# Performance work log

Hardware: AMD Instinct MI355X
Metric: run time of the kernel (lower is better)

The kernel has to match this reference:

```python
import jax, jax.numpy as jnp
import numpy as np

B, L, C, H, K, P = 64, 2048, 128, 128, 64, 336
NUM_BLOCKS = 4
EPS = 1e-5


def _revin_norm(x):
    mean = jnp.mean(x, axis=1, keepdims=True)
    std = jnp.sqrt(jnp.var(x, axis=1, keepdims=True) + EPS)
    return (x - mean) / std, mean, std


def _bn(x, gamma, beta, ch_axis):
    # training-mode BatchNorm1d: stats over all axes except ch_axis
    axes = tuple(i for i in range(x.ndim) if i != ch_axis)
    mean = jnp.mean(x, axis=axes, keepdims=True)
    var = jnp.var(x, axis=axes, keepdims=True)
    shp = [1] * x.ndim
    shp[ch_axis] = -1
    return (x - mean) / jnp.sqrt(var + EPS) * gamma.reshape(shp) + beta.reshape(shp)


def _mixer_block(x, bn_t_g, bn_t_b, lin_t_w, lin_t_b, bn_f_g, bn_f_b,
                 lin_f1_w, lin_f1_b, lin_f2_w, lin_f2_b):
    # timestep mixer: BN treats seq dim as channels, Linear over seq dim
    y = _bn(x, bn_t_g, bn_t_b, 1)                       # [B,L,C]
    y = jnp.swapaxes(y, 1, 2)                           # [B,C,L]
    y = jax.nn.gelu(y @ lin_t_w + lin_t_b, approximate=False)
    y = jnp.swapaxes(y, 1, 2)
    x = x + y
    # feature mixer: BN over channel dim, 2-layer MLP over features
    y = jnp.swapaxes(x, 1, 2)                           # [B,C,L]
    y = _bn(y, bn_f_g, bn_f_b, 1)
    y = jnp.swapaxes(y, 1, 2)                           # [B,L,C]
    y = jax.nn.gelu(y @ lin_f1_w + lin_f1_b, approximate=False)
    y = y @ lin_f2_w + lin_f2_b
    return x + y


def _forward(x, bern_u, cluster_embeds, wq_w, wq_b, wk_w, wk_b, wv_w, wv_b,
             cm_w1, cm_b1, cm_w2, cm_b2, tm_w1, tm_b1, tm_w2, tm_b2,
             bn_t_g, bn_t_b, lin_t_w, lin_t_b, bn_f_g, bn_f_b,
             lin_f1_w, lin_f1_b, lin_f2_w, lin_f2_b, out_w, out_b):
    xn, _, _ = _revin_norm(x)                           # [B,L,C]
    # channel MLP -> token embeddings h_i
    h = jax.nn.relu(xn @ cm_w1 + cm_b1) @ cm_w2 + cm_b2  # [B,L,H]
    # cosine-similarity soft routing to codebook
    hn = h / (jnp.linalg.norm(h, axis=-1, keepdims=True) + 1e-8)
    cn = cluster_embeds / (jnp.linalg.norm(cluster_embeds, axis=-1, keepdims=True) + 1e-8)
    p = jax.nn.softmax(jnp.einsum('blh,kh->blk', hn, cn), axis=-1)   # [B,L,K]
    M = (bern_u < p).astype(x.dtype)                    # bernoulli sample via external uniforms
    # exp-attention between cluster queries and token keys, masked by M
    Q = cluster_embeds @ wq_w + wq_b                    # [K,H]
    Km = h @ wk_w + wk_b                                # [B,L,H]
    V = h @ wv_w + wv_b                                 # [B,L,H]
    scores = jnp.einsum('kh,blh->bkl', Q, Km) / jnp.sqrt(jnp.asarray(H, x.dtype))
    aw = jax.nn.softmax(jnp.exp(scores) * jnp.swapaxes(M, 1, 2), axis=-1)  # [B,K,L]
    ao = jnp.einsum('bkl,blh->bkh', aw, V)              # [B,K,H]
    upd = ao * jnp.mean(p, axis=1)[:, :, None]          # prob-weighted cluster update
    new_cluster_embeds = jnp.mean(upd, axis=0)          # [K,H] (EMA-style copy target)
    # temporal module on channel embeddings
    h2 = jax.nn.relu(h @ tm_w1 + tm_b1) @ tm_w2 + tm_b2  # [B,L,H], H==C
    z, mean2, std2 = _revin_norm(h2)                    # second 'norm' overwrites stats
    for _ in range(NUM_BLOCKS):
        z = _mixer_block(z, bn_t_g, bn_t_b, lin_t_w, lin_t_b,
                         bn_f_g, bn_f_b, lin_f1_w, lin_f1_b, lin_f2_w, lin_f2_b)
    y = jnp.swapaxes(jnp.swapaxes(z, 1, 2) @ out_w + out_b, 1, 2)    # [B,P,C]
    y = y * std2 + mean2                                # denorm with second-call stats
    return y, new_cluster_embeds


def setup_inputs() -> dict:
    key = jax.random.key(0)
    ks = iter(jax.random.split(key, 40))

    def lin_w(fan_in, shape):
        return jax.random.uniform(next(ks), shape, jnp.float32, -1.0, 1.0) / np.sqrt(fan_in).astype(np.float32)

    return {
        'x': jax.random.normal(next(ks), (B, L, C), jnp.float32),
        'bern_u': jax.random.uniform(next(ks), (B, L, K), jnp.float32),
        'cluster_embeds': jax.random.normal(next(ks), (K, H), jnp.float32),
        'wq_w': lin_w(H, (H, H)), 'wq_b': lin_w(H, (H,)),
        'wk_w': lin_w(H, (H, H)), 'wk_b': lin_w(H, (H,)),
        'wv_w': lin_w(H, (H, H)), 'wv_b': lin_w(H, (H,)),
        'cm_w1': lin_w(C, (C, H)), 'cm_b1': lin_w(C, (H,)),
        'cm_w2': lin_w(H, (H, H)), 'cm_b2': lin_w(H, (H,)),
        'tm_w1': lin_w(H, (H, H)), 'tm_b1': lin_w(H, (H,)),
        'tm_w2': lin_w(H, (H, H)), 'tm_b2': lin_w(H, (H,)),
        'bn_t_g': jnp.ones((L,), jnp.float32), 'bn_t_b': jnp.zeros((L,), jnp.float32),
        'lin_t_w': lin_w(L, (L, L)), 'lin_t_b': lin_w(L, (L,)),
        'bn_f_g': jnp.ones((C,), jnp.float32), 'bn_f_b': jnp.zeros((C,), jnp.float32),
        'lin_f1_w': lin_w(C, (C, H)), 'lin_f1_b': lin_w(C, (H,)),
        'lin_f2_w': lin_w(H, (H, C)), 'lin_f2_b': lin_w(H, (C,)),
        'out_w': lin_w(L, (L, P)), 'out_b': lin_w(L, (P,)),
    }


def reference(x, bern_u, cluster_embeds, wq_w, wq_b, wk_w, wk_b, wv_w, wv_b,
              cm_w1, cm_b1, cm_w2, cm_b2, tm_w1, tm_b1, tm_w2, tm_b2,
              bn_t_g, bn_t_b, lin_t_w, lin_t_b, bn_f_g, bn_f_b,
              lin_f1_w, lin_f1_b, lin_f2_w, lin_f2_b, out_w, out_b):
    return _forward(x, bern_u, cluster_embeds, wq_w, wq_b, wk_w, wk_b, wv_w, wv_b,
                    cm_w1, cm_b1, cm_w2, cm_b2, tm_w1, tm_b1, tm_w2, tm_b2,
                    bn_t_g, bn_t_b, lin_t_w, lin_t_b, bn_f_g, bn_f_b,
                    lin_f1_w, lin_f1_b, lin_f2_w, lin_f2_b, out_w, out_b)
```

## Files before the change

kernel.cpp:

```cpp
#include <hip/hip_runtime.h>
#include <math.h>

#define BB 64
#define LL 2048
#define CC 128
#define HH 128
#define KK 64
#define PP 336
#define EPSf 1e-5f

typedef __attribute__((ext_vector_type(8))) short short8v;
typedef __attribute__((ext_vector_type(4))) float float4v;

__device__ inline ushort f2bf(float f) {
    union { float f; unsigned u; } v; v.f = f;
    unsigned r = (v.u + 0x7FFFu + ((v.u >> 16) & 1u)) >> 16;
    return (ushort)r;
}
__device__ inline float bf2f(ushort h) {
    union { unsigned u; float f; } v; v.u = ((unsigned)h) << 16;
    return v.f;
}

__device__ inline float fast_gelu(float v) {
// ... 283 lines not shown
    __shared__ ushort Xlo[PREC ? 128 : 1][72];
    __shared__ ushort Bh[128][72];
    __shared__ ushort Bl[PREC ? 128 : 1][72];
    int tid = threadIdx.x;
    int m0 = blockIdx.x * 128;
    int noff = (NORM == 1) ? (m0 / LL) * normStride : 0;
    int w = tid >> 6, lane = tid & 63;
    int wm = (w >> 1) * 64, wn = (w & 1) * 64;
    int col = lane & 15, kq = lane >> 4;

    float4v acc[4][4];
    #pragma unroll
    for (int i = 0; i < 4; ++i)
        #pragma unroll
        for (int j = 0; j < 4; ++j) acc[i][j] = (float4v){0.f, 0.f, 0.f, 0.f};

    for (int kt = 0; kt < 2; ++kt) {
        __syncthreads();
        #pragma unroll
        for (int it = 0; it < 4; ++it) {
            int q = tid + it * 256;
            int row = q >> 3, k0 = (q & 7) * 8;
            int kg = kt * 64 + k0;
            const float* ap = A + (size_t)(m0 + row) * 128 + kg;
            float vv[8];
            *(float4*)&vv[0] = *(const float4*)ap;
            *(float4*)&vv[4] = *(const float4*)(ap + 4);
            ushort hi[8], lo[8];
            #pragma unroll
            for (int j = 0; j < 8; ++j) {
                float v = vv[j];
                if (NORM == 1) v = (v - nmu[noff + kg + j]) * ns[noff + kg + j];
                if (NORM == 2) v = (v - nmu[kg + j]) * ns[kg + j] + nt[kg + j];
                ushort h = f2bf(v);
                hi[j] = h;
                if (PREC) lo[j] = f2bf(v - bf2f(h));
            }
            *(short8v*)&Xhi[row][k0] = *(short8v*)hi;
            if (PREC) *(short8v*)&Xlo[row][k0] = *(short8v*)lo;
        }
        #pragma unroll
        for (int it = 0; it < 4; ++it) {
            int q = tid + it * 256;
            int row = q >> 3, k0 = (q & 7) * 8;
            *(short8v*)&Bh[row][k0] =
                *(const short8v*)(W1h + (size_t)row * 128 + kt * 64 + k0);
            if (PREC)
                *(short8v*)&Bl[row][k0] =
                    *(const short8v*)(W1l + (size_t)row * 128 + kt * 64 + k0);
        }
        __syncthreads();
        #pragma unroll
        for (int ksub = 0; ksub < 2; ++ksub) {
            short8v ah[4], al[4], bh[4], bl[4];
            #pragma unroll
            for (int mf = 0; mf < 4; ++mf) {
                ah[mf] = *(const short8v*)&Xhi[wm + mf * 16 + col][ksub * 32 + kq * 8];
                if (PREC) al[mf] = *(const short8v*)&Xlo[wm + mf * 16 + col][ksub * 32 + kq * 8];
            }
            #pragma unroll
            for (int nf = 0; nf < 4; ++nf) {
                bh[nf] = *(const short8v*)&Bh[wn + nf * 16 + col][ksub * 32 + kq * 8];
                if (PREC) bl[nf] = *(const short8v*)&Bl[wn + nf * 16 + col][ksub * 32 + kq * 8];
            }
            #pragma unroll
            for (int mf = 0; mf < 4; ++mf)
                #pragma unroll
                for (int nf = 0; nf < 4; ++nf)
                    acc[mf][nf] = __builtin_amdgcn_mfma_f32_16x16x32_bf16(
                        ah[mf], bh[nf], acc[mf][nf], 0, 0, 0);
            if (PREC) {
                #pragma unroll
                for (int mf = 0; mf < 4; ++mf)
                    #pragma unroll
                    for (int nf = 0; nf < 4; ++nf)
                        acc[mf][nf] = __builtin_amdgcn_mfma_f32_16x16x32_bf16(
                            ah[mf], bl[nf], acc[mf][nf], 0, 0, 0);
                #pragma unroll
                for (int mf = 0; mf < 4; ++mf)
                    #pragma unroll
                    for (int nf = 0; nf < 4; ++nf)
                        acc[mf][nf] = __builtin_amdgcn_mfma_f32_16x16x32_bf16(
                            al[mf], bh[nf], acc[mf][nf], 0, 0, 0);
            }
        }
    }

    float4v acc2[4][4];
    #pragma unroll
    for (int i = 0; i < 4; ++i)
        #pragma unroll
        for (int j = 0; j < 4; ++j) acc2[i][j] = (float4v){0.f, 0.f, 0.f, 0.f};

    for (int kt2 = 0; kt2 < 2; ++kt2) {
        __syncthreads();
        if ((wn >> 6) == kt2) {
            #pragma unroll
            for (int nf = 0; nf < 4; ++nf) {
                float bn = b1v[wn + nf * 16 + col];
                #pragma unroll
                for (int mf = 0; mf < 4; ++mf) {
                    #pragma unroll
                    for (int r = 0; r < 4; ++r) {
                        float v = acc[mf][nf][r] + bn;
                        if (ACT1 == 1) v = fmaxf(v, 0.f);
                        if (ACT1 == 2) v = fast_gelu(v);
                        int row = wm + mf * 16 + kq * 4 + r;
                        int c2 = nf * 16 + col;
                        ushort h = f2bf(v);
                        Xhi[row][c2] = h;
                        if (PREC) Xlo[row][c2] = f2bf(v - bf2f(h));
                    }
                }
            }
        }
        #pragma unroll
        for (int it = 0; it < 4; ++it) {
            int q = tid + it * 256;
            int row = q >> 3, k0 = (q & 7) * 8;
            *(short8v*)&Bh[row][k0] =
                *(const short8v*)(W2h + (size_t)row * 128 + kt2 * 64 + k0);
            if (PREC)
                *(short8v*)&Bl[row][k0] =
                    *(const short8v*)(W2l + (size_t)row * 128 + kt2 * 64 + k0);
        }
        __syncthreads();
        #pragma unroll
        for (int ksub = 0; ksub < 2; ++ksub) {
            short8v ah[4], al[4], bh[4], bl[4];
            #pragma unroll
            for (int mf = 0; mf < 4; ++mf) {
                ah[mf] = *(const short8v*)&Xhi[wm + mf * 16 + col][ksub * 32 + kq * 8];
                if (PREC) al[mf] = *(const short8v*)&Xlo[wm + mf * 16 + col][ksub * 32 + kq * 8];
            }
            #pragma unroll
            for (int nf = 0; nf < 4; ++nf) {
                bh[nf] = *(const short8v*)&Bh[wn + nf * 16 + col][ksub * 32 + kq * 8];
                if (PREC) bl[nf] = *(const short8v*)&Bl[wn + nf * 16 + col][ksub * 32 + kq * 8];
            }
            #pragma unroll
            for (int mf = 0; mf < 4; ++mf)
                #pragma unroll
                for (int nf = 0; nf < 4; ++nf)
                    acc2[mf][nf] = __builtin_amdgcn_mfma_f32_16x16x32_bf16(
                        ah[mf], bh[nf], acc2[mf][nf], 0, 0, 0);
            if (PREC) {
                #pragma unroll
                for (int mf = 0; mf < 4; ++mf)
                    #pragma unroll
                    for (int nf = 0; nf < 4; ++nf)
                        acc2[mf][nf] = __builtin_amdgcn_mfma_f32_16x16x32_bf16(
                            ah[mf], bl[nf], acc2[mf][nf], 0, 0, 0);
                #pragma unroll
                for (int mf = 0; mf < 4; ++mf)
                    #pragma unroll
                    for (int nf = 0; nf < 4; ++nf)
                        acc2[mf][nf] = __builtin_amdgcn_mfma_f32_16x16x32_bf16(
                            al[mf], bh[nf], acc2[mf][nf], 0, 0, 0);
            }
        }
    }

    int rbase = kq * 4;
    float rs_[4][4];
    float rq_[4][4];
    float cs_[4], cq_[4];
    if (EP2 == 1 || EP2 == 3) {
        #pragma unroll
        for (int a = 0; a < 4; ++a)
            #pragma unroll
            for (int b = 0; b < 4; ++b) { rs_[a][b] = 0.f; rq_[a][b] = 0.f; }
    }
    if (EP2 == 2) {
        #pragma unroll
        for (int a = 0; a < 4; ++a) { cs_[a] = 0.f; cq_[a] = 0.f; }
    }
    #pragma unroll
    for (int nf = 0; nf < 4; ++nf) {
        int n = wn + nf * 16 + col;
        float bn = b2v[n];
        #pragma unroll
        for (int mf = 0; mf < 4; ++mf) {
            #pragma unroll
            for (int r = 0; r < 4; ++r) {
                int m = m0 + wm + mf * 16 + rbase + r;
                float v = acc2[mf][nf][r] + bn;
                if (ACT2 == 1) v = fmaxf(v, 0.f);
                if (ACT2 == 2) v = fast_gelu(v);
                if (EP2 == 1) {
                    float fin = Out[(size_t)m * 128 + n] + v;
                    Out[(size_t)m * 128 + n] = fin;
                    rs_[mf][r] += fin;
                    rq_[mf][r] += fin * fin;
                } else {
                    Out[(size_t)m * 128 + n] = v;
                    if (EP2 == 2) { cs_[nf] += v; cq_[nf] += v * v; }
                    if (EP2 == 3) rq_[mf][r] += v * v;
                }
            }
        }
    }
    if (EP2 == 1) {
        #pragma unroll
        for (int mf = 0; mf < 4; ++mf)
            #pragma unroll
            for (int r = 0; r < 4; ++r) {
                float s = rs_[mf][r], q = rq_[mf][r];
                #pragma unroll
                for (int o = 1; o <= 8; o <<= 1) {
                    s += __shfl_xor(s, o);
                    q += __shfl_xor(q, o);
                }
                rs_[mf][r] = s; rq_[mf][r] = q;
            }
        __syncthreads();
        float* sred = (float*)&Xhi[0][0];
        float* qred = sred + 256;
        if (col == 0) {
            #pragma unroll
            for (int mf = 0; mf < 4; ++mf)
                #pragma unroll
                for (int r = 0; r < 4; ++r) {
                    int row = wm + mf * 16 + kq * 4 + r;
                    sred[row * 2 + (wn >> 6)] = rs_[mf][r];
                    qred[row * 2 + (wn >> 6)] = rq_[mf][r];
                }
        }
        __syncthreads();
        if (tid < 128) {
            rsum[(size_t)m0 + tid] = sred[tid * 2] + sred[tid * 2 + 1];
            rsq[(size_t)m0 + tid]  = qred[tid * 2] + qred[tid * 2 + 1];
        }
    }
    if (EP2 == 3) {
        #pragma unroll
        for (int mf = 0; mf < 4; ++mf)
            #pragma unroll
            for (int r = 0; r < 4; ++r) {
                float q = rq_[mf][r];
                #pragma unroll
                for (int o = 1; o <= 8; o <<= 1) q += __shfl_xor(q, o);
                rq_[mf][r] = q;
            }
        __syncthreads();
        float* qred = (float*)&Xhi[0][0];
        if (col == 0) {
            #pragma unroll
            for (int mf = 0; mf < 4; ++mf)
                #pragma unroll
                for (int r = 0; r < 4; ++r) {
                    int row = wm + mf * 16 + kq * 4 + r;
                    qred[row * 2 + (wn >> 6)] = rq_[mf][r];
                }
        }
        __syncthreads();
        if (tid < 128)
            rsq[(size_t)m0 + tid] = qred[tid * 2] + qred[tid * 2 + 1];
    }
    if (EP2 == 2) {
        #pragma unroll
        for (int nf = 0; nf < 4; ++nf) {
            #pragma unroll
            for (int o = 16; o <= 32; o <<= 1) {
                cs_[nf] += __shfl_xor(cs_[nf], o);
                cq_[nf] += __shfl_xor(cq_[nf], o);
            }
        }
        __syncthreads();
        float* colS = (float*)&Xhi[0][0];
        float* colQ = colS + 256;
        if (kq == 0) {
            #pragma unroll
            for (int nf = 0; nf < 4; ++nf) {
                int n = wn + nf * 16 + col;
                colS[(wm >> 6) * 128 + n] = cs_[nf];
                colQ[(wm >> 6) * 128 + n] = cq_[nf];
            }
        }
        __syncthreads();
        if (tid < 128) {
            rsum[(size_t)blockIdx.x * 256 + tid] = colS[tid] + colS[128 + tid];
            rsum[(size_t)blockIdx.x * 256 + 128 + tid] = colQ[tid] + colQ[128 + tid];
        }
    }
}

__global__ void wsplit_kernel(const float* __restrict__ W, ushort* __restrict__ Whi,
                              ushort* __restrict__ Wlo) {
    __shared__ float t[32][33];
    int k0 = blockIdx.x * 32, n0 = blockIdx.y * 32;
    int tx = threadIdx.x, ty = threadIdx.y;
    for (int i = ty; i < 32; i += 8)
        t[i][tx] = W[(size_t)(k0 + i) * 128 + n0 + tx];
    __syncthreads();
    for (int i = ty; i < 32; i += 8) {
        float v = t[tx][i];
        ushort h = f2bf(v);
        Whi[(size_t)(n0 + i) * 128 + k0 + tx] = h;
        Wlo[(size_t)(n0 + i) * 128 + k0 + tx] = f2bf(v - bf2f(h));
    }
}

__global__ __launch_bounds__(512, 1)
void mfma_ts2_kernel(const ushort* __restrict__ A, const ushort* __restrict__ W,
                     const float* __restrict__ bias, float* Z,
                     float* __restrict__ bnfP) {
    extern __shared__ __align__(16) ushort smem2[];
    float (*Ol)[260] = (float(*)[260])smem2;

    int bid = blockIdx.x;
    int swz = (bid & 7) * 32 + (bid >> 3);
    int n0 = (swz & 7) * 256;
    int m0 = (swz >> 3) * 256;

    int tid = threadIdx.x;
    int w = tid >> 6, lane = tid & 63;
    int wm = (w >> 2) * 128, wn = (w & 3) * 64;
    int col = lane & 15, kq = lane >> 4;
    int srow = lane >> 3;
    int scol = ((lane & 7) ^ srow) << 3;
    int xr = (col & 7) << 4;

    float4v acc[8][4];
    #pragma unroll
    for (int i = 0; i < 8; ++i)
        #pragma unroll
        for (int j = 0; j < 4; ++j) acc[i][j] = (float4v){0.f, 0.f, 0.f, 0.f};

    const int kTiles = 32;
    auto stage = [&](int kt2, int bsel) {
        ushort* Ab = smem2 + bsel * 32768;
        ushort* Bb = Ab + 16384;
        int kb = kt2 << 6;
        #pragma unroll
        for (int it = 0; it < 4; ++it) {
            int rb = w * 32 + it * 8;
            async16(A + (size_t)(m0 + rb + srow) * LL + kb + scol, Ab + (rb << 6));
            async16(W + (size_t)(n0 + rb + srow) * LL + kb + scol, Bb + (rb << 6));
        }
    };

    stage(0, 0);
    __syncthreads();
    for (int kt = 0; kt < kTiles; ++kt) {
        int cur = kt & 1;
        const ushort* Ac = smem2 + cur * 32768;
        const ushort* Bc = Ac + 16384;
        if (kt + 1 < kTiles) stage(kt + 1, cur ^ 1);
        __builtin_amdgcn_s_setprio(1);
        #pragma unroll
        for (int ksub = 0; ksub < 2; ++ksub) {
            int cswz = (((ksub << 6) + (kq << 4)) ^ xr) >> 1;
            short8v af[8], bf[4];
            #pragma unroll
            for (int mf = 0; mf < 8; ++mf)
                af[mf] = *(const short8v*)(Ac + (wm + mf * 16 + col) * 64 + cswz);
            #pragma unroll
            for (int nf = 0; nf < 4; ++nf)
                bf[nf] = *(const short8v*)(Bc + (wn + nf * 16 + col) * 64 + cswz);
            #pragma unroll
            for (int mf = 0; mf < 8; ++mf)
                #pragma unroll
                for (int nf = 0; nf < 4; ++nf)
                    acc[mf][nf] = __builtin_amdgcn_mfma_f32_16x16x32_bf16(
                        af[mf], bf[nf], acc[mf][nf], 0, 0, 0);
        }
        __builtin_amdgcn_s_setprio(0);
        __syncthreads();
    }

    int b0 = m0 >> 7;
    float cs[16], cq[16];
    #pragma unroll
    for (int j = 0; j < 16; ++j) { cs[j] = 0.f; cq[j] = 0.f; }
    int nloc = tid >> 4, c0 = (tid & 15) * 16;
    int bb = b0 + (c0 >> 7);
    int ccc = c0 & 127;
    #pragma unroll
    for (int q = 0; q < 8; ++q) {
        __syncthreads();
        #pragma unroll
        for (int nf = 0; nf < 4; ++nf) {
            int gnl = wn + nf * 16;
            if ((gnl >> 5) != q) continue;
            int gn = n0 + gnl + col;
            float bn = bias[gn];
            int nl = gnl - q * 32 + col;
            #pragma unroll
            for (int mf = 0; mf < 8; ++mf)
                #pragma unroll
                for (int r = 0; r < 4; ++r) {
                    float v = acc[mf][nf][r] + bn;
                    v = fast_gelu(v);
                    Ol[nl][wm + mf * 16 + kq * 4 + r] = v;
                }
        }
        __syncthreads();
        int gn = n0 + q * 32 + nloc;
        float* zr = Z + ((size_t)bb * LL + gn) * CC + ccc;
        #pragma unroll
        for (int i = 0; i < 4; ++i) {
            float4 v = *(float4*)&Ol[nloc][c0 + i * 4];
            float4 o = *(float4*)(zr + i * 4);
            v.x += o.x; v.y += o.y; v.z += o.z; v.w += o.w;
            *(float4*)(zr + i * 4) = v;
            cs[i * 4 + 0] += v.x; cs[i * 4 + 1] += v.y;
            cs[i * 4 + 2] += v.z; cs[i * 4 + 3] += v.w;
            cq[i * 4 + 0] += v.x * v.x; cq[i * 4 + 1] += v.y * v.y;
            cq[i * 4 + 2] += v.z * v.z; cq[i * 4 + 3] += v.w * v.w;
        }
    }
    __syncthreads();
    float* sred = (float*)smem2;
    float* qred = sred + 8192;
    #pragma unroll
    for (int j = 0; j < 16; ++j) {
        sred[nloc * 256 + c0 + j] = cs[j];
        qred[nloc * 256 + c0 + j] = cq[j];
    }
    __syncthreads();
    if (tid < 128) {
        float a = 0.f;
        for (int r = 0; r < 32; ++r)
            a += sred[r * 256 + tid] + sred[r * 256 + 128 + tid];
        bnfP[(size_t)bid * 256 + tid] = a;
    } else if (tid < 256) {
        int c = tid - 128;
        float a = 0.f;
        for (int r = 0; r < 32; ++r)
            a += qred[r * 256 + c] + qred[r * 256 + 128 + c];
        bnfP[(size_t)bid * 256 + 128 + c] = a;
    }
}

template <int EPM>
__global__ __launch_bounds__(256)
void mfma_gemm_kernel(const ushort* __restrict__ A, const ushort* __restrict__ W,
                      const float* __restrict__ bias, float* Z,
                      int N, int Kd, int LDO, int nx, int nwg,
                      const float* __restrict__ epS, const float* __restrict__ epM,
                      float* __restrict__ bnfP) {
    __shared__ __align__(16) ushort smem[32768];
    float (*Ol)[132] = (float(*)[132])smem;

    int bid = blockIdx.x;
    int cpx = nwg >> 3;
    int swz = (bid & 7) * cpx + (bid >> 3);
    int n0 = (swz % nx) * 128;
    int m0 = (swz / nx) * 128;

    int tid = threadIdx.x;
    int w = tid >> 6, lane = tid & 63;
    int wm = (w >> 1) * 64, wn = (w & 1) * 64;
    int col = lane & 15, kq = lane >> 4;

    int srow = lane >> 3;
    int scol = ((lane & 7) ^ srow) << 3;
    int xr = (col & 7) << 4;

    float4v acc[4][4];
    #pragma unroll
    for (int i = 0; i < 4; ++i)
        #pragma unroll
        for (int j = 0; j < 4; ++j) acc[i][j] = (float4v){0.f, 0.f, 0.f, 0.f};

    int kTiles = Kd >> 6;

    #pragma unroll
    for (int it = 0; it < 4; ++it) {
        int rb = (w << 5) + (it << 3);
        async16(A + (size_t)(m0 + rb + srow) * Kd + scol, smem + (rb << 6));
    }
    #pragma unroll
    for (int it = 0; it < 4; ++it) {
        int rb = (w << 5) + (it << 3);
        async16(W + (size_t)(n0 + rb + srow) * Kd + scol, smem + 8192 + (rb << 6));
    }
    __syncthreads();

    for (int kt = 0; kt < kTiles; ++kt) {
        int cur = kt & 1;
        ushort* Ac = smem + (cur << 14);
        ushort* Bc = Ac + 8192;
        if (kt + 1 < kTiles) {
            ushort* An = smem + ((cur ^ 1) << 14);
            ushort* Bn = An + 8192;
            int kb = (kt + 1) << 6;
            #pragma unroll
            for (int it = 0; it < 4; ++it) {
                int rb = (w << 5) + (it << 3);
                async16(A + (size_t)(m0 + rb + srow) * Kd + kb + scol, An + (rb << 6));
            }
            #pragma unroll
            for (int it = 0; it < 4; ++it) {
                int rb = (w << 5) + (it << 3);
                async16(W + (size_t)(n0 + rb + srow) * Kd + kb + scol, Bn + (rb << 6));
            }
        }
        __builtin_amdgcn_s_setprio(1);
        #pragma unroll
        for (int ksub = 0; ksub < 2; ++ksub) {
            int cswz = (((ksub << 6) + (kq << 4)) ^ xr) >> 1;
            short8v af[4], bf[4];
            #pragma unroll
            for (int mf = 0; mf < 4; ++mf)
                af[mf] = *(const short8v*)(Ac + (wm + mf * 16 + col) * 64 + cswz);
            #pragma unroll
            for (int nf = 0; nf < 4; ++nf)
                bf[nf] = *(const short8v*)(Bc + (wn + nf * 16 + col) * 64 + cswz);
            #pragma unroll
            for (int mf = 0; mf < 4; ++mf)
                #pragma unroll
                for (int nf = 0; nf < 4; ++nf)
                    acc[mf][nf] = __builtin_amdgcn_mfma_f32_16x16x32_bf16(
                        af[mf], bf[nf], acc[mf][nf], 0, 0, 0);
        }
        __builtin_amdgcn_s_setprio(0);
        __syncthreads();
    }

    int b = m0 >> 7;
    float cs[16], cq[16];
    if (EPM == 1) {
        #pragma unroll
        for (int k2 = 0; k2 < 16; ++k2) { cs[k2] = 0.f; cq[k2] = 0.f; }
    }
    #pragma unroll
    for (int q = 0; q < 4; ++q) {
        __syncthreads();
        #pragma unroll
        for (int nf = 0; nf < 4; ++nf) {
            int gnl = wn + nf * 16;
            if ((gnl >> 5) != q) continue;
            int gn = n0 + gnl + col;
            float bn = (EPM == 2 && gn >= N) ? 0.f : bias[gn];
            int nl = gnl - q * 32 + col;
            #pragma unroll
            for (int mf = 0; mf < 4; ++mf) {
                #pragma unroll
                for (int r = 0; r < 4; ++r) {
                    float v = acc[mf][nf][r] + bn;
                    if (EPM == 1) v = fast_gelu(v);
                    Ol[nl][wm + mf * 16 + kq * 4 + r] = v;
                }
            }
        }
        __syncthreads();
        int nloc = tid >> 3, c0 = (tid & 7) * 16;
        int gn = n0 + q * 32 + nloc;
        if ((EPM == 2 || EPM == 3) && gn >= N) continue;
        float* zr;
        if (EPM == 3)
            zr = Z + (((size_t)(m0 >> 11) * 64 + gn) * 2048) + (m0 & 2047) + c0;
        else
            zr = Z + ((size_t)b * LDO + gn) * CC + c0;
        #pragma unroll
        for (int i = 0; i < 4; ++i) {
            float4 v = *(float4*)&Ol[nloc][c0 + i * 4];
            if (EPM == 1) {
                float4 o = *(float4*)(zr + i * 4);
                v.x += o.x; v.y += o.y; v.z += o.z; v.w += o.w;
                *(float4*)(zr + i * 4) = v;
                cs[i * 4 + 0] += v.x; cs[i * 4 + 1] += v.y;
                cs[i * 4 + 2] += v.z; cs[i * 4 + 3] += v.w;
                cq[i * 4 + 0] += v.x * v.x; cq[i * 4 + 1] += v.y * v.y;
                cq[i * 4 + 2] += v.z * v.z; cq[i * 4 + 3] += v.w * v.w;
            } else if (EPM == 2) {
                int mb = m0 + c0 + i * 4;
                float4 s4 = *(const float4*)(epS + mb);
                float4 m4 = *(const float4*)(epM + mb);
                v.x = v.x * s4.x + m4.x; v.y = v.y * s4.y + m4.y;
                v.z = v.z * s4.z + m4.z; v.w = v.w * s4.w + m4.w;
                *(float4*)(zr + i * 4) = v;
            } else {
                *(float4*)(zr + i * 4) = v;
            }
        }
    }
    if (EPM == 1) {
        __syncthreads();
        float* sred = (float*)smem;
        float* qred = sred + 4096;
        int rrow = tid >> 3, cb = (tid & 7) * 16;
        #pragma unroll
        for (int k2 = 0; k2 < 16; ++k2) {
            sred[rrow * 128 + cb + k2] = cs[k2];
            qred[rrow * 128 + cb + k2] = cq[k2];
        }
        __syncthreads();
        if (tid < 128) {
            float a = 0.f;
            for (int r = 0; r < 32; ++r) a += sred[r * 128 + tid];
            bnfP[(size_t)bid * 256 + tid] = a;
        } else {
            int c = tid - 128;
            float a = 0.f;
            for (int r = 0; r < 32; ++r) a += qred[r * 128 + c];
            bnfP[(size_t)bid * 256 + 128 + c] = a;
        }
    }
}

__global__ void wtrans_kernel(const float* __restrict__ W, ushort* __restrict__ WT,
                              int Kd, int N) {
    __shared__ float t[32][33];
    int k0 = blockIdx.x * 32, n0 = blockIdx.y * 32;
    int tx = threadIdx.x, ty = threadIdx.y;
    for (int i = ty; i < 32; i += 8) {
        int n = n0 + tx;
        t[i][tx] = (n < N) ? W[(size_t)(k0 + i) * N + n] : 0.f;
    }
    __syncthreads();
    for (int i = ty; i < 32; i += 8)
        WT[(size_t)(n0 + i) * Kd + k0 + tx] = f2bf(t[tx][i]);
}

__global__ void cn_split_kernel(const float* __restrict__ ce, ushort* __restrict__ ch,
                                ushort* __restrict__ cl) {
    int k = blockIdx.x, h = threadIdx.x;
    if (k >= KK) {
        ch[(size_t)k * 128 + h] = 0;
        cl[(size_t)k * 128 + h] = 0;
        return;
    }
    __shared__ float sh[128];
    float v = ce[(size_t)k * HH + h];
    sh[h] = v * v;
    __syncthreads();
    for (int o = 64; o >= 1; o >>= 1) {
        if (h < o) sh[h] += sh[h + o];
        __syncthreads();
    }
    float nv = v / (sqrtf(sh[0]) + 1e-8f);
    ushort hh = f2bf(nv);
    ch[(size_t)k * 128 + h] = hh;
    cl[(size_t)k * 128 + h] = f2bf(nv - bf2f(hh));
}

__global__ void qprime_kernel(const float* __restrict__ Q, const float* __restrict__ wk_w,
                              const float* __restrict__ wk_b, ushort* __restrict__ qpb,
                              float* __restrict__ qbp) {
    int k = blockIdx.x;
    int hp = threadIdx.x;
    if (k >= KK) {
        qpb[(size_t)k * HH + hp] = 0;
        if (hp == 0) qbp[k] = 0.f;
        return;
    }
    __shared__ float qrow[128];
    __shared__ float red[128];
    qrow[hp] = Q[(size_t)k * HH + hp];
    __syncthreads();
    float s = 0.f;
    for (int h = 0; h < HH; ++h) s = fmaf(qrow[h], wk_w[(size_t)hp * HH + h], s);
    const float rs = 0.088388347648318447f;
    qpb[(size_t)k * HH + hp] = f2bf(s * rs);
    red[hp] = qrow[hp] * wk_b[hp];
    __syncthreads();
    for (int o = 64; o >= 1; o >>= 1) {
        if (hp < o) red[hp] += red[hp + o];
        __syncthreads();
    }
    if (hp == 0) qbp[k] = red[0] * rs;
}

__global__ __launch_bounds__(256)
void pmask_kernel(const float* __restrict__ sp, const float* __restrict__ rn,
                  const float* __restrict__ bern, unsigned char* __restrict__ Mt,
                  float* __restrict__ ppart) {
    int b = blockIdx.y;
    int l0 = blockIdx.x * 32;
// ... 38 lines not shown
__global__ __launch_bounds__(256)
void aw_kernel(float* __restrict__ S, const unsigned char* __restrict__ Mt) {
    size_t base = (size_t)blockIdx.x * LL;
    int tid = threadIdx.x;
    float t[8];
    float mx = -1e30f;
    #pragma unroll
    for (int i = 0; i < 8; ++i) {
        int l = tid + i * 256;
        float v = expf(S[base + l]) * (float)Mt[base + l];
        t[i] = v;
        mx = fmaxf(mx, v);
    }
    __shared__ float shA[4];
    __shared__ float shB[4];
    #pragma unroll
    for (int o = 32; o >= 1; o >>= 1) mx = fmaxf(mx, __shfl_xor(mx, o));
    if ((tid & 63) == 0) shA[tid >> 6] = mx;
    __syncthreads();
    mx = fmaxf(fmaxf(shA[0], shA[1]), fmaxf(shA[2], shA[3]));
    float e[8];
    float sum = 0.f;
    #pragma unroll
    for (int i = 0; i < 8; ++i) { e[i] = expf(t[i] - mx); sum += e[i]; }
    #pragma unroll
    for (int o = 32; o >= 1; o >>= 1) sum += __shfl_xor(sum, o);
    if ((tid & 63) == 0) shB[tid >> 6] = sum;
    __syncthreads();
    sum = (shB[0] + shB[1]) + (shB[2] + shB[3]);
    float inv = 1.f / sum;
    #pragma unroll
    for (int i = 0; i < 8; ++i) S[base + tid + i * 256] = e[i] * inv;
}

__global__ __launch_bounds__(256)
void awh_part_kernel(const float* __restrict__ AWs, const float* __restrict__ hmat,
                     float* __restrict__ part) {
    __shared__ float AT[32][64];
    __shared__ float VT[32][128];
    int b = blockIdx.y, sp = blockIdx.x;
    int tid = threadIdx.x;
    int tx = tid & 15, ty = tid >> 4;
    float acc[4][8] = {};
    const float* Ab = AWs + (size_t)b * KK * LL + sp * 512;
    const float* Vb = hmat + ((size_t)b * LL + sp * 512) * HH;
    for (int lt = 0; lt < 512; lt += 32) {
        __syncthreads();
        #pragma unroll
        for (int it = 0; it < 2; ++it) {
            int q = tid + it * 256;
            int row = q >> 3;
            int lq = (q & 7) << 2;
            float4 v = *(const float4*)(Ab + (size_t)row * LL + lt + lq);
            AT[lq][row] = v.x; AT[lq + 1][row] = v.y;
            AT[lq + 2][row] = v.z; AT[lq + 3][row] = v.w;
        }
        #pragma unroll
        for (int it = 0; it < 4; ++it) {
            int q = tid + it * 256;
            int lr = q >> 5;
            int hc = (q & 31) << 2;
            *(float4*)&VT[lr][hc] = *(const float4*)(Vb + (size_t)(lt + lr) * HH + hc);
        }
        __syncthreads();
        #pragma unroll
        for (int l = 0; l < 32; ++l) {
            float av[4], vv[8];
            *(float4*)&av[0] = *(const float4*)&AT[l][ty * 4];
            *(float4*)&vv[0] = *(const float4*)&VT[l][tx * 4];
            *(float4*)&vv[4] = *(const float4*)&VT[l][64 + tx * 4];
            #pragma unroll
            for (int i = 0; i < 4; ++i)
                #pragma unroll
                for (int j = 0; j < 8; ++j)
                    acc[i][j] = fmaf(av[i], vv[j], acc[i][j]);
        }
    }
    #pragma unroll
    for (int i = 0; i < 4; ++i) {
        int k = ty * 4 + i;
        #pragma unroll
        for (int jj = 0; jj < 8; jj += 4) {
            int h = (jj ? 64 + tx * 4 : tx * 4);
            float o[4];
            #pragma unroll
            for (int j = 0; j < 4; ++j) o[j] = acc[i][jj + j];
            *(float4*)(part + (((size_t)b * 4 + sp) * KK + k) * HH + h) = *(float4*)o;
        }
    }
}

__global__ void awh_reduce_kernel(const float* __restrict__ part, float* __restrict__ awh) {
    int bk = blockIdx.x, h = threadIdx.x;
    int b = bk >> 6, k = bk & 63;
    float s = 0.f;
    #pragma unroll
    for (int sp = 0; sp < 4; ++sp)
        s += part[(((size_t)b * 4 + sp) * KK + k) * HH + h];
    awh[(size_t)bk * HH + h] = s;
}

__global__ void newce_kernel(const float* __restrict__ ao, const float* __restrict__ pm,
                             float* __restrict__ outTail) {
    int k = blockIdx.x, h = threadIdx.x;
    float s = 0.f;
    for (int b = 0; b < BB; ++b)
        s += ao[((size_t)b * KK + k) * HH + h] * pm[b * KK + k];
    outTail[(size_t)k * HH + h] = s * (1.f / BB);
}

__global__ void revin_apply_kernel(const float* __restrict__ in, float* __restrict__ out,
                                   const float* __restrict__ mu, const float* __restrict__ rs,
                                   float* __restrict__ rsum, float* __restrict__ rsq) {
    int b = blockIdx.y;
    size_t base = (size_t)b * LL * CC + (size_t)blockIdx.x * 8192;
    int c0 = (threadIdx.x * 4) & 127;
    int lane = threadIdx.x & 63;
    float4 m4 = *(const float4*)(mu + b * CC + c0);
    float4 r4 = *(const float4*)(rs + b * CC + c0);
    #pragma unroll
    for (int j = 0; j < 8; ++j) {
        float4 v = *(const float4*)(in + base + threadIdx.x * 4 + j * 1024);
        v.x = (v.x - m4.x) * r4.x; v.y = (v.y - m4.y) * r4.y;
        v.z = (v.z - m4.z) * r4.z; v.w = (v.w - m4.w) * r4.w;
        *(float4*)(out + base + threadIdx.x * 4 + j * 1024) = v;
        float s = v.x + v.y + v.z + v.w;
        float q = v.x * v.x + v.y * v.y + v.z * v.z + v.w * v.w;
        #pragma unroll
        for (int o = 1; o <= 16; o <<= 1) {
            s += __shfl_xor(s, o);
            q += __shfl_xor(q, o);
        }
        if ((lane & 31) == 0) {
            size_t row = (base + (size_t)threadIdx.x * 4 + (size_t)j * 1024) >> 7;
            rsum[row] = s;
            rsq[row] = q;
        }
    }
}

__global__ void bnt_final_kernel(const float* __restrict__ rsum, const float* __restrict__ rsq,
                                 float* __restrict__ mu, float* __restrict__ rv) {
    int l = blockIdx.x * 256 + threadIdx.x;
    float s = 0.f, q = 0.f;
    for (int b = 0; b < BB; ++b) {
        s += rsum[(size_t)b * LL + l];
        q += rsq[(size_t)b * LL + l];
    }
    float m = s * (1.f / (BB * CC));
    float var = q * (1.f / (BB * CC)) - m * m;
    var = fmaxf(var, 0.f);
    mu[l] = m;
    rv[l] = 1.f / sqrtf(var + EPSf);
}

template <bool DO_BN>
__global__ __launch_bounds__(256)
void transpose_bn_kernel(const float* __restrict__ in, ushort* __restrict__ out,
                         const float* __restrict__ mu, const float* __restrict__ rv,
                         const float* __restrict__ g, const float* __restrict__ be) {
    __shared__ ushort tile[32][72];
    int l0 = blockIdx.x * 64, c0 = blockIdx.y * 32, b = blockIdx.z;
    int t = threadIdx.x;
    const float* ib = in + ((size_t)b * LL + l0) * CC + c0;
    #pragma unroll
    for (int it = 0; it < 2; ++it) {
        int idx = t + it * 256;
        int row = idx >> 3;
        int c = (idx & 7) * 4;
        float4 v = *(const float4*)(ib + (size_t)row * CC + c);
        if (DO_BN) {
            int l = l0 + row;
            float sc = rv[l] * g[l];
            float m = mu[l], bb = be[l];
            v.x = (v.x - m) * sc + bb; v.y = (v.y - m) * sc + bb;
            v.z = (v.z - m) * sc + bb; v.w = (v.w - m) * sc + bb;
        }
        tile[c    ][row] = f2bf(v.x);
        tile[c + 1][row] = f2bf(v.y);
        tile[c + 2][row] = f2bf(v.z);
        tile[c + 3][row] = f2bf(v.w);
    }
    __syncthreads();
    int cc = t >> 3, l8 = (t & 7) * 8;
    ushort* ob = out + (size_t)b * CC * LL + (size_t)(c0 + cc) * LL + l0 + l8;
    *(uint4*)ob = *(const uint4*)&tile[cc][l8];
}

__global__ void bnf_mid_kernel(const float* __restrict__ part, float* __restrict__ mid,
                               int cnt) {
    int gblk = blockIdx.x, t = threadIdx.x;
    float s = 0.f;
    for (int i = 0; i < cnt; ++i)
        s += part[(size_t)(gblk * cnt + i) * 256 + t];
    mid[(size_t)gblk * 256 + t] = s;
}

__global__ void bnf_final_kernel(const float* __restrict__ mid, const float* __restrict__ g,
                                 const float* __restrict__ be, float* __restrict__ mu,
                                 float* __restrict__ sA, float* __restrict__ tA) {
    int c = threadIdx.x;
    float s = 0.f, s2 = 0.f;
    #pragma unroll
    for (int i = 0; i < 64; ++i) {
        s += mid[(size_t)i * 256 + c];
        s2 += mid[(size_t)i * 256 + 128 + c];
    }
    float m = s / (float)(BB * LL);
    float var = s2 / (float)(BB * LL) - m * m;
    var = fmaxf(var, 0.f);
    float rvv = 1.f / sqrtf(var + EPSf);
    mu[c] = m;
    sA[c] = rvv * g[c];
    tA[c] = be[c];
}

extern "C" void kernel_launch(void* const* d_in, const int* in_sizes, int n_in,
                              void* d_out, int out_size, void* d_ws, size_t ws_size,
                              hipStream_t stream) {
    const float* x     = (const float*)d_in[0];
    const float* bern  = (const float*)d_in[1];
    const float* ce    = (const float*)d_in[2];
    const float* wq_w  = (const float*)d_in[3];
    const float* wq_b  = (const float*)d_in[4];
    const float* wk_w  = (const float*)d_in[5];
    const float* wk_b  = (const float*)d_in[6];
    const float* wv_w  = (const float*)d_in[7];
    const float* wv_b  = (const float*)d_in[8];
    const float* cm_w1 = (const float*)d_in[9];
    const float* cm_b1 = (const float*)d_in[10];
    const float* cm_w2 = (const float*)d_in[11];
    const float* cm_b2 = (const float*)d_in[12];
    const float* tm_w1 = (const float*)d_in[13];
    const float* tm_b1 = (const float*)d_in[14];
    const float* tm_w2 = (const float*)d_in[15];
    const float* tm_b2 = (const float*)d_in[16];
    const float* bn_t_g = (const float*)d_in[17];
    const float* bn_t_b = (const float*)d_in[18];
    const float* lin_t_w = (const float*)d_in[19];
    const float* lin_t_b = (const float*)d_in[20];
    const float* bn_f_g = (const float*)d_in[21];
    const float* bn_f_b = (const float*)d_in[22];
    const float* f1_w  = (const float*)d_in[23];
    const float* f1_b  = (const float*)d_in[24];
    const float* f2_w  = (const float*)d_in[25];
    const float* f2_b  = (const float*)d_in[26];
    const float* out_w = (const float*)d_in[27];
    const float* out_b = (const float*)d_in[28];
    (void)in_sizes; (void)n_in; (void)out_size;

    float* y = (float*)d_out;
    float* ceOut = y + (size_t)BB * PP * CC;

    float* ws = (float*)d_ws;
    size_t off = 0;
    auto alloc = [&](size_t n) { float* p = ws + off; off += n; return p; };
    float* mean1  = alloc(BB * CC);
    float* rstd1  = alloc(BB * CC);
    float* std1   = alloc(BB * CC);
    float* mean2  = alloc(BB * CC);
    float* rstd2  = alloc(BB * CC);
    float* std2   = alloc(BB * CC);
    float* bnmu   = alloc(LL);
    float* bnrv   = alloc(LL);
    float* bfpart = alloc(1024 * 256);
    float* bfmid  = alloc(64 * 256);
    float* bfmu   = alloc(CC);
    float* bfs    = alloc(CC);
    float* bft    = alloc(CC);
    float* cxpart = alloc(BB * 8 * 256);
    float* cpart2 = alloc(1024 * 256);
    float* qbuf   = alloc(KK * HH);
    ushort* qpb   = (ushort*)alloc(128 * 128 / 2);
    float* qbp    = alloc(128);
    ushort* cnbh  = (ushort*)alloc(8192);
    ushort* cnbl  = (ushort*)alloc(8192);
    float* rn     = alloc((size_t)BB * LL);
    float* rsum   = alloc((size_t)BB * LL);
    float* rsq    = alloc((size_t)BB * LL);
    float* ppart  = alloc((size_t)BB * (LL / 32) * KK);
    float* pmean  = alloc(BB * KK);
    float* awhprt = alloc((size_t)BB * 4 * KK * HH);
    float* awh    = alloc((size_t)BB * KK * HH);
    float* aobuf  = alloc((size_t)BB * KK * HH);
    ushort* wsp   = (ushort*)alloc(7 * 2 * 16384 / 2);
    ushort* wtT   = (ushort*)alloc((size_t)LL * LL / 2);
    ushort* owT   = (ushort*)alloc((size_t)384 * LL / 2);
    float* S      = alloc((size_t)BB * KK * LL);
    float* buf0   = alloc((size_t)BB * LL * CC);
    float* buf2   = alloc((size_t)BB * LL * CC);
    unsigned char* Mt = (unsigned char*)(ws + off);
    ushort* abf = (ushort*)S;
    ushort* hb  = (ushort*)buf0;
    (void)ws_size;

    auto whi = [&](int i) { return wsp + (size_t)i * 2 * 16384; };
    auto wlo = [&](int i) { return wsp + (size_t)i * 2 * 16384 + 16384; };

    const int ML = BB * LL;
    dim3 tb(32, 8);
    dim3 tgrid(LL / 64, CC / 32, BB);
    dim3 wsg(4, 4);

    bool useTs2 =
        (hipFuncSetAttribute((const void*)mfma_ts2_kernel,
                             hipFuncAttributeMaxDynamicSharedMemorySize,
                             131072) == hipSuccess);

    wtrans_kernel<<<dim3(LL / 32, LL / 32), tb, 0, stream>>>(lin_t_w, wtT, LL, LL);
    wtrans_kernel<<<dim3(LL / 32, 12), tb, 0, stream>>>(out_w, owT, LL, PP);
    wsplit_kernel<<<wsg, tb, 0, stream>>>(cm_w1, whi(0), wlo(0));
    wsplit_kernel<<<wsg, tb, 0, stream>>>(cm_w2, whi(1), wlo(1));
    wsplit_kernel<<<wsg, tb, 0, stream>>>(tm_w1, whi(2), wlo(2));
    wsplit_kernel<<<wsg, tb, 0, stream>>>(tm_w2, whi(3), wlo(3));
    wsplit_kernel<<<wsg, tb, 0, stream>>>(f1_w, whi(4), wlo(4));
    wsplit_kernel<<<wsg, tb, 0, stream>>>(f2_w, whi(5), wlo(5));
    wsplit_kernel<<<wsg, tb, 0, stream>>>(wv_w, whi(6), wlo(6));

    colstats_part_kernel<<<dim3(8, BB), 256, 0, stream>>>(x, cxpart);
    colstats_final_kernel<<<dim3(BB), dim3(128), 0, stream>>>(cxpart, mean1, rstd1, std1);
    mfma_sq2_kernel<1, 1, 0, 3, 1><<<dim3(ML / 128), 256, 0, stream>>>(
        x, whi(0), wlo(0), cm_b1, whi(1), wlo(1), cm_b2, buf2, mean1, rstd1, nullptr, CC,
        nullptr, rsq);
    rn_final_kernel<<<dim3(ML / 256), 256, 0, stream>>>(rsq, rn);
    gemm_kernel<<<dim3(1, 1), 256, 0, stream>>>(ce, wq_w, wq_b, qbuf,
        KK, HH, HH, HH, HH, HH);
    qprime_kernel<<<dim3(128), dim3(128), 0, stream>>>(qbuf, wk_w, wk_b, qpb, qbp);
    cn_split_kernel<<<dim3(128), dim3(128), 0, stream>>>(ce, cnbh, cnbl);
    mfma_sq_kernel<0, 0, 2><<<dim3(ML / 128), 256, 0, stream>>>(
        buf2, cnbh, cnbl, nullptr, S, nullptr, nullptr, nullptr, 0, hb);
    pmask_kernel<<<dim3(LL / 32, BB), 256, 0, stream>>>(S, rn, bern, Mt, ppart);
    pmean_final_kernel<<<dim3(BB), dim3(64), 0, stream>>>(ppart, pmean);
    mfma_gemm_kernel<3><<<dim3(1024), 256, 0, stream>>>(
        hb, qpb, qbp, S, KK, 128, 0, 1, 1024, nullptr, nullptr, nullptr);
    aw_kernel<<<dim3(BB * KK), 256, 0, stream>>>(S, Mt);
    awh_part_kernel<<<dim3(4, BB), 256, 0, stream>>>(S, buf2, awhprt);
    awh_reduce_kernel<<<dim3(BB * KK), dim3(128), 0, stream>>>(awhprt, awh);
    mfma_sq_kernel<0, 0, 0><<<dim3((BB * KK) / 128), 256, 0, stream>>>(
        awh, whi(6), wlo(6), wv_b, aobuf, nullptr, nullptr, nullptr, 0, nullptr);
    newce_kernel<<<dim3(KK), dim3(128), 0, stream>>>(aobuf, pmean, ceOut);
    mfma_sq2_kernel<0, 1, 0, 2, 1><<<dim3(ML / 128), 256, 0, stream>>>(
        buf2, whi(2), wlo(2), tm_b1, whi(3), wlo(3), tm_b2, buf0,
        nullptr, nullptr, nullptr, 0, cpart2, nullptr);
    colstats2_final_kernel<<<dim3(BB), dim3(128), 0, stream>>>(cpart2, mean2, rstd2, std2);
    revin_apply_kernel<<<dim3(32, BB), 256, 0, stream>>>(buf0, buf2, mean2, rstd2, rsum, rsq);
    for (int blkI = 0; blkI < 4; ++blkI) {
        bnt_final_kernel<<<dim3(8), 256, 0, stream>>>(rsum, rsq, bnmu, bnrv);
        transpose_bn_kernel<true><<<tgrid, 256, 0, stream>>>(buf2, abf, bnmu, bnrv, bn_t_g, bn_t_b);
        if (useTs2) {
            mfma_ts2_kernel<<<dim3(256), 512, 131072, stream>>>(
                abf, wtT, lin_t_b, buf2, bfpart);
            bnf_mid_kernel<<<dim3(64), 256, 0, stream>>>(bfpart, bfmid, 4);
        } else {
            mfma_gemm_kernel<1><<<dim3(1024), 256, 0, stream>>>(
                abf, wtT, lin_t_b, buf2, LL, LL, LL, 16, 1024, nullptr, nullptr, bfpart);
            bnf_mid_kernel<<<dim3(64), 256, 0, stream>>>(bfpart, bfmid, 16);
        }
        bnf_final_kernel<<<dim3(1), dim3(128), 0, stream>>>(bfmid, bn_f_g, bn_f_b, bfmu, bfs, bft);
        mfma_sq2_kernel<2, 2, 0, 1, 0><<<dim3(ML / 128), 256, 0, stream>>>(
            buf2, whi(4), wlo(4), f1_b, whi(5), wlo(5), f2_b, buf2, bfmu, bfs, bft, 0,
            rsum, rsq);
    }
    transpose_bn_kernel<false><<<tgrid, 256, 0, stream>>>(buf2, abf,
        nullptr, nullptr, nullptr, nullptr);
    mfma_gemm_kernel<2><<<dim3(192), 256, 0, stream>>>(
        abf, owT, out_b, y, PP, LL, PP, 3, 192, std2, mean2, nullptr);
}
```

Measured before the change: 1.357 ms.

## Use 4-stage async pipeline with half-k tiles in time-mixing GEMM

Restructures the main timestep-mixing GEMM mainloop from a double-buffered 64-wide k tile into a four-slot ring of 32-wide k stages, kept three stages ahead, with explicit vmcnt waits and a single barrier per stage. It also changes the LDS layout to pack two rows per 64-element line with a new XOR swizzle, so fragment reads avoid bank conflicts. The aim is to hide global-load latency better and drop the trailing __syncthreads. The risk is that it relies on exact vmcnt counting and a ring-slot reuse distance for correctness.

```diff
diff --git a/kernel.cpp b/kernel.cpp
--- a/kernel.cpp
+++ b/kernel.cpp
@@ -609,7 +609,7 @@
 }
 
 __global__ __launch_bounds__(512, 1)
-void mfma_ts2_kernel(const ushort* __restrict__ A, const ushort* __restrict__ W,
+void mfma_ts3_kernel(const ushort* __restrict__ A, const ushort* __restrict__ W,
                      const float* __restrict__ bias, float* Z,
                      float* __restrict__ bnfP) {
     extern __shared__ __align__(16) ushort smem2[];
@@ -624,9 +624,15 @@
     int w = tid >> 6, lane = tid & 63;
     int wm = (w >> 2) * 128, wn = (w & 3) * 64;
     int col = lane & 15, kq = lane >> 4;
-    int srow = lane >> 3;
-    int scol = ((lane & 7) ^ srow) << 3;
-    int xr = (col & 7) << 4;
+
+    int l3 = lane >> 3;
+    int u0 = (lane & 7) ^ l3;
+    int urow = l3 * 2 + (u0 >> 2);
+    int ucol = (u0 & 3) * 8;
+
+    int uoff = ((((col & 1) << 2) | kq) ^ (col >> 1)) * 8;
+    int rA2b = (wm >> 1) + (col >> 1);
+    int rB2b = (wn >> 1) + (col >> 1);
 
     float4v acc[8][4];
     #pragma unroll
@@ -634,46 +640,44 @@
         #pragma unroll
         for (int j = 0; j < 4; ++j) acc[i][j] = (float4v){0.f, 0.f, 0.f, 0.f};
 
-    const int kTiles = 32;
-    auto stage = [&](int kt2, int bsel) {
-        ushort* Ab = smem2 + bsel * 32768;
-        ushort* Bb = Ab + 16384;
-        int kb = kt2 << 6;
-        #pragma unroll
-        for (int it = 0; it < 4; ++it) {
-            int rb = w * 32 + it * 8;
-            async16(A + (size_t)(m0 + rb + srow) * LL + kb + scol, Ab + (rb << 6));
-            async16(W + (size_t)(n0 + rb + srow) * LL + kb + scol, Bb + (rb << 6));
+    auto stage = [&](int q) {
+        int kb = (q >> 1) * 64 + (q & 1) * 32;
+        ushort* base = smem2 + (q & 3) * 16384;
+        #pragma unroll
+        for (int it = 0; it < 2; ++it) {
+            int R0 = w * 16 + it * 8;
+            async16(A + (size_t)(m0 + R0 * 2 + urow) * LL + kb + ucol,
+                    base + R0 * 64);
+            async16(W + (size_t)(n0 + R0 * 2 + urow) * LL + kb + ucol,
+                    base + 8192 + R0 * 64);
         }
     };
 
-    stage(0, 0);
-    __syncthreads();
-    for (int kt = 0; kt < kTiles; ++kt) {
-        int cur = kt & 1;
-        const ushort* Ac = smem2 + cur * 32768;
-        const ushort* Bc = Ac + 16384;
-        if (kt + 1 < kTiles) stage(kt + 1, cur ^ 1);
+    stage(0); stage(1); stage(2);
+
+    for (int P = 0; P < 64; ++P) {
+        if (P < 62)       asm volatile("s_waitcnt vmcnt(8)" ::: "memory");
+        else if (P == 62) asm volatile("s_waitcnt vmcnt(4)" ::: "memory");
+        else              asm volatile("s_waitcnt vmcnt(0)" ::: "memory");
+        __builtin_amdgcn_s_barrier();
+        __builtin_amdgcn_sched_barrier(0);
+        if (P < 61) stage(P + 3);
+        const ushort* base = smem2 + (size_t)(P & 3) * 16384;
+        short8v af[8], bf4[4];
+        #pragma unroll
+        for (int mf = 0; mf < 8; ++mf)
+            af[mf] = *(const short8v*)(base + (rA2b + mf * 8) * 64 + uoff);
+        #pragma unroll
+        for (int nf = 0; nf < 4; ++nf)
+            bf4[nf] = *(const short8v*)(base + 8192 + (rB2b + nf * 8) * 64 + uoff);
         __builtin_amdgcn_s_setprio(1);
         #pragma unroll
-        for (int ksub = 0; ksub < 2; ++ksub) {
-            int cswz = (((ksub << 6) + (kq << 4)) ^ xr) >> 1;
-            short8v af[8], bf[4];
-            #pragma unroll
-            for (int mf = 0; mf < 8; ++mf)
-                af[mf] = *(const short8v*)(Ac + (wm + mf * 16 + col) * 64 + cswz);
+        for (int mf = 0; mf < 8; ++mf)
             #pragma unroll
             for (int nf = 0; nf < 4; ++nf)
-                bf[nf] = *(const short8v*)(Bc + (wn + nf * 16 + col) * 64 + cswz);
-            #pragma unroll
-            for (int mf = 0; mf < 8; ++mf)
-                #pragma unroll
-                for (int nf = 0; nf < 4; ++nf)
-                    acc[mf][nf] = __builtin_amdgcn_mfma_f32_16x16x32_bf16(
-                        af[mf], bf[nf], acc[mf][nf], 0, 0, 0);
-        }
+                acc[mf][nf] = __builtin_amdgcn_mfma_f32_16x16x32_bf16(
+                    af[mf], bf4[nf], acc[mf][nf], 0, 0, 0);
         __builtin_amdgcn_s_setprio(0);
-        __syncthreads();
     }
 
     int b0 = m0 >> 7;
@@ -1318,8 +1322,8 @@
     dim3 tgrid(LL / 64, CC / 32, BB);
     dim3 wsg(4, 4);
 
-    bool useTs2 =
-        (hipFuncSetAttribute((const void*)mfma_ts2_kernel,
+    bool useTs3 =
+        (hipFuncSetAttribute((const void*)mfma_ts3_kernel,
                              hipFuncAttributeMaxDynamicSharedMemorySize,
                              131072) == hipSuccess);
 
@@ -1363,8 +1367,8 @@
     for (int blkI = 0; blkI < 4; ++blkI) {
         bnt_final_kernel<<<dim3(8), 256, 0, stream>>>(rsum, rsq, bnmu, bnrv);
         transpose_bn_kernel<true><<<tgrid, 256, 0, stream>>>(buf2, abf, bnmu, bnrv, bn_t_g, bn_t_b);
-        if (useTs2) {
-            mfma_ts2_kernel<<<dim3(256), 512, 131072, stream>>>(
+        if (useTs3) {
+            mfma_ts3_kernel<<<dim3(256), 512, 131072, stream>>>(
                 abf, wtT, lin_t_b, buf2, bfpart);
             bnf_mid_kernel<<<dim3(64), 256, 0, stream>>>(bfpart, bfmid, 4);
         } else {
```

New measurement: 1.370 ms. About the same (+1.0%).
